# Kernel optimization log

Measured on AMD Instinct MI355X. Metric: run time of the kernel, lower is better.

Reference implementation:

```python
import jax, jax.numpy as jnp
import numpy as np

# Mamba2 dims (defaults: expand=2, d_state=128, d_conv=4, ngroups=1)
D_MODEL = 1024
HEADDIM = 64
D_STATE = 128
D_CONV = 4
D_INNER = 2 * D_MODEL            # 2048
NHEADS = D_INNER // HEADDIM      # 32
CONV_DIM = D_INNER + 2 * D_STATE # 2304
D_IN_PROJ = 2 * D_INNER + 2 * D_STATE + NHEADS  # 4384
EPS = 1e-5


def setup_inputs() -> dict:
    key = jax.random.key(0)
    ks = jax.random.split(key, 12)
    B, L = 4, 2048
    inp = {}
    inp['query'] = jax.random.normal(ks[0], (B, L, D_MODEL), jnp.float32)
    inp['key'] = jax.random.normal(ks[1], (B, L, D_MODEL), jnp.float32)
    inp['value'] = jax.random.normal(ks[2], (B, L, D_MODEL), jnp.float32)
    # parameters (Mamba2-style init)
    inp['in_proj_w'] = jax.random.normal(ks[3], (D_IN_PROJ, D_MODEL), jnp.float32) * (D_MODEL ** -0.5)
    inp['conv_w'] = jax.random.normal(ks[4], (CONV_DIM, D_CONV), jnp.float32) * (D_CONV ** -0.5)
    inp['conv_b'] = jnp.zeros((CONV_DIM,), jnp.float32)
    # dt init: softplus^{-1}(dt) with dt ~ U[1e-3, 1e-1]
    dt = jnp.exp(jax.random.uniform(ks[5], (NHEADS,)) * (np.log(0.1) - np.log(1e-3)) + np.log(1e-3))
    inp['dt_bias'] = dt + jnp.log(-jnp.expm1(-dt))
    # A ~ U[1, 16], A_log = log(A)
    inp['A_log'] = jnp.log(jax.random.uniform(ks[6], (NHEADS,), minval=1.0, maxval=16.0))
    inp['D'] = jnp.ones((NHEADS,), jnp.float32)
    inp['norm_w'] = jnp.ones((D_INNER,), jnp.float32)
    inp['out_proj_w'] = jax.random.normal(ks[7], (D_MODEL, D_INNER), jnp.float32) * (D_INNER ** -0.5)
    return inp


def _mamba2_forward(u, in_proj_w, conv_w, conv_b, dt_bias, A_log, D, norm_w, out_proj_w):
    b, l, _ = u.shape
    zxbcdt = jnp.einsum('bld,ed->ble', u, in_proj_w)  # (b,l,D_IN_PROJ)
    z = zxbcdt[..., :D_INNER]
    xBC = zxbcdt[..., D_INNER:D_INNER + CONV_DIM]
    dt = jax.nn.softplus(zxbcdt[..., -NHEADS:] + dt_bias)  # (b,l,h)
    # depthwise causal conv1d over time, kernel D_CONV, + silu
    xBC_pad = jnp.pad(xBC, ((0, 0), (D_CONV - 1, 0), (0, 0)))
    conv = conv_b
    for k in range(D_CONV):
        conv = conv + xBC_pad[:, k:k + l, :] * conv_w[:, k]
    xBC = jax.nn.silu(conv)
    x = xBC[..., :D_INNER].reshape(b, l, NHEADS, HEADDIM)   # (b,l,h,p)
    Bm = xBC[..., D_INNER:D_INNER + D_STATE]                # (b,l,n) ngroups=1
    Cm = xBC[..., D_INNER + D_STATE:]                       # (b,l,n)
    A = -jnp.exp(A_log)                                      # (h,)
    dA = jnp.exp(dt * A)                                     # (b,l,h)

    def step(h, inputs):
        dA_t, dt_t, x_t, B_t, C_t = inputs  # (b,h),(b,h),(b,h,p),(b,n),(b,n)
        h = h * dA_t[:, :, None, None] + (dt_t[:, :, None, None] * x_t[..., None]) * B_t[:, None, None, :]
        y = jnp.einsum('bhpn,bn->bhp', h, C_t)
        return h, y

    h0 = jnp.zeros((b, NHEADS, HEADDIM, D_STATE), u.dtype)
    xs = (dA.transpose(1, 0, 2), dt.transpose(1, 0, 2), x.transpose(1, 0, 2, 3),
          Bm.transpose(1, 0, 2), Cm.transpose(1, 0, 2))
    _, ys = jax.lax.scan(step, h0, xs)
    y = ys.transpose(1, 0, 2, 3) + x * D[None, None, :, None]  # (b,l,h,p)
    y = y.reshape(b, l, D_INNER)
    # RMSNormGated (norm_before_gate=False): norm(y * silu(z)) * w
    y = y * jax.nn.silu(z)
    y = y * jax.lax.rsqrt(jnp.mean(y * y, axis=-1, keepdims=True) + EPS) * norm_w
    return jnp.einsum('ble,de->bld', y, out_proj_w)


def reference(query, key, value, in_proj_w, conv_w, conv_b, dt_bias, A_log, D, norm_w, out_proj_w):
    # wrapper ignores key/value; returns mamba(query) (cache pass-through omitted)
    return _mamba2_forward(query, in_proj_w, conv_w, conv_b, dt_bias, A_log, D, norm_w, out_proj_w)
```

## Files before the change

### kernel.cpp

```cpp
#include <hip/hip_runtime.h>
#include <hip/hip_bf16.h>


typedef __attribute__((ext_vector_type(8))) short bf16x8;
typedef __attribute__((ext_vector_type(4))) float f32x4;

static constexpr int B_ = 4;
static constexpr int L_ = 2048;
static constexpr int NROWS = B_ * L_;
static constexpr int DMODEL = 1024;
static constexpr int DINNER = 2048;
static constexpr int NH = 32;
static constexpr int DSTATE = 128;
static constexpr int CONVDIM = DINNER + 2 * DSTATE;
static constexpr int DINPROJ = 2 * DINNER + 2 * DSTATE + NH;
static constexpr int Q_ = 64;
static constexpr int NCHUNK = L_ / Q_;

__device__ __forceinline__ unsigned pk_bf16(float a, float b) {
  unsigned ua = __builtin_bit_cast(unsigned, a);
  unsigned ub = __builtin_bit_cast(unsigned, b);
  ua = (ua + 0x7FFFu + ((ua >> 16) & 1u)) >> 16;
  ub = (ub + 0x7FFFu + ((ub >> 16) & 1u)) >> 16;
  return (ua & 0xFFFFu) | (ub << 16);
}
__device__ __forceinline__ unsigned short bf16_of(float a) {
  unsigned ua = __builtin_bit_cast(unsigned, a);
  return (unsigned short)((ua + 0x7FFFu + ((ua >> 16) & 1u)) >> 16);
}
__device__ __forceinline__ float f_of_bf16(unsigned short s) {
  return __builtin_bit_cast(float, (unsigned)s << 16);
}
__device__ __forceinline__ unsigned short* state_slot(unsigned short* lo,
                                                      unsigned short* hi,
                                                      int bh, int c) {
  int i = bh * NCHUNK + c;
  return (i < 2048) ? lo + (size_t)i * 8192 : hi + (size_t)(i - 2048) * 8192;
}

__global__ __launch_bounds__(256) void cast4_kernel(const float* __restrict__ in,
                                                    unsigned short* __restrict__ out) {
  int i = blockIdx.x * 256 + threadIdx.x;
  float4 v = ((const float4*)in)[i];
  ((uint2*)out)[i] = make_uint2(pk_bf16(v.x, v.y), pk_bf16(v.z, v.w));
}

#define WAITVM(N) asm volatile("s_waitcnt vmcnt(" #N ")" ::: "memory")

template <bool C_BF16>
__global__ __launch_bounds__(512, 2) void gemm256_kernel(
    const unsigned short* __restrict__ A, const unsigned short* __restrict__ Bw,
    void* __restrict__ Cp, int M, int N, int K, int lda, int ldb, int ldc) {
  (void)M;
  __shared__ unsigned short sA[4 * 256 * 32];
  __shared__ unsigned short sB[4 * 256 * 32];
  const int tid = threadIdx.x;
  const int w = tid >> 6;
  const int lane = tid & 63;
  const int quad = lane >> 4;
  const int r15 = lane & 15;

  const int NT = gridDim.x;
  const int nwg = NT * gridDim.y;
  const int orig = blockIdx.y * NT + blockIdx.x;
  const int qq = nwg >> 3, rm = nwg & 7;
  const int xcd = orig & 7, loc = orig >> 3;
  const int id = (xcd < rm ? xcd * (qq + 1) : rm * (qq + 1) + (xcd - rm) * qq) + loc;
  const int m0 = (id / NT) << 8;
  const int n0 = (id % NT) << 8;

  const int wm = w >> 2;
  const int wn = w & 3;

  const int srow = lane >> 2;
  const int sch = lane & 3;
  const int row0 = w * 32 + srow;
  const int row1 = row0 + 16;
  const int ca0 = (sch ^ ((row0 >> 1) & 3)) * 8;
  const int ca1 = (sch ^ ((row1 >> 1) & 3)) * 8;
  const int nslice = K >> 5;

  f32x4 acc[8][4];
#pragma unroll
  for (int i = 0; i < 8; ++i)
#pragma unroll
    for (int j = 0; j < 4; ++j) acc[i][j] = f32x4{0.f, 0.f, 0.f, 0.f};

  auto ldsA = (__attribute__((address_space(3))) unsigned short*)sA;
  auto ldsB = (__attribute__((address_space(3))) unsigned short*)sB;

  auto stage = [&](int ks) {
    const int so = (ks & 3) * 8192 + w * 1024;
    const unsigned short* ga = A + (size_t)(m0 + row0) * lda + ks * 32;
    const unsigned short* gb = Bw + (size_t)(n0 + row0) * ldb + ks * 32;
    __builtin_amdgcn_global_load_lds(
        (const __attribute__((address_space(1))) void*)(ga + ca0),
        (__attribute__((address_space(3))) void*)(ldsA + so), 16, 0, 0);
    __builtin_amdgcn_global_load_lds(
        (const __attribute__((address_space(1))) void*)(gb + ca0),
        (__attribute__((address_space(3))) void*)(ldsB + so), 16, 0, 0);
    __builtin_amdgcn_global_load_lds(
        (const __attribute__((address_space(1))) void*)(ga + (size_t)16 * lda + ca1),
        (__attribute__((address_space(3))) void*)(ldsA + so + 512), 16, 0, 0);
    __builtin_amdgcn_global_load_lds(
        (const __attribute__((address_space(1))) void*)(gb + (size_t)16 * ldb + ca1),
        (__attribute__((address_space(3))) void*)(ldsB + so + 512), 16, 0, 0);
  };

  stage(0);
  stage(1);
  stage(2);
  WAITVM(8);
  __builtin_amdgcn_s_barrier();

  const int kx = (quad ^ ((r15 >> 1) & 3)) * 8;
  int s = 0;

#define GPHASE(STAGE_STMT, WTN)                                                \
  {                                                                            \
    const unsigned short* pa = sA + (s & 3) * 8192;                            \
    const unsigned short* pb = sB + (s & 3) * 8192;                            \
    bf16x8 af[8], bfv[4];                                                      \
    _Pragma("unroll") for (int i = 0; i < 8; ++i)                              \
        af[i] = *(const bf16x8*)&pa[(wm * 128 + i * 16 + r15) * 32 + kx];      \
    _Pragma("unroll") for (int j = 0; j < 4; ++j)                              \
        bfv[j] = *(const bf16x8*)&pb[(wn * 64 + j * 16 + r15) * 32 + kx];      \
    STAGE_STMT;                                                                \
    WAITVM(WTN);                                                               \
    __builtin_amdgcn_s_barrier();                                              \
    __builtin_amdgcn_s_setprio(1);                                             \
    _Pragma("unroll") for (int i = 0; i < 8; ++i)                              \
        _Pragma("unroll") for (int j = 0; j < 4; ++j)                          \
            acc[i][j] = __builtin_amdgcn_mfma_f32_16x16x32_bf16(               \
                af[i], bfv[j], acc[i][j], 0, 0, 0);                            \
    __builtin_amdgcn_s_setprio(0);                                             \
    __builtin_amdgcn_s_barrier();                                              \
  }

  for (; s < nslice - 3; ++s) GPHASE(stage(s + 3), 8);
  GPHASE((void)0, 4);
  ++s;
  GPHASE((void)0, 0);
  ++s;
  GPHASE((void)0, 0);
#undef GPHASE

  const int rq = quad * 4;
#pragma unroll
  for (int i = 0; i < 8; ++i) {
#pragma unroll
    for (int j = 0; j < 4; ++j) {
      int gcol = n0 + wn * 64 + j * 16 + r15;
      if (gcol < N) {
#pragma unroll
        for (int r = 0; r < 4; ++r) {
          size_t grow = (size_t)(m0 + wm * 128 + i * 16 + rq + r);
          if constexpr (C_BF16)
            ((unsigned short*)Cp)[grow * (size_t)ldc + gcol] = bf16_of(acc[i][j][r]);
          else
            ((float*)Cp)[grow * (size_t)ldc + gcol] = acc[i][j][r];
        }
      }
    }
  }
}

__global__ __launch_bounds__(256) void conv_kernel(const unsigned short* __restrict__ zx,
                                                   const float* __restrict__ conv_w,
                                                   const float* __restrict__ conv_b,
                                                   unsigned short* __restrict__ xbc) {
  int c = blockIdx.x * 256 + threadIdx.x;
  int row = blockIdx.y;
  int l = row & (L_ - 1);
  float acc = conv_b[c];
#pragma unroll
  for (int k = 0; k < 4; ++k) {
    int ll = l + k - 3;
    if (ll >= 0)
      acc = fmaf(f_of_bf16(zx[(size_t)(row + k - 3) * DINPROJ + DINNER + c]),
                 conv_w[c * 4 + k], acc);
  }
  acc = acc / (1.f + __expf(-acc));
  xbc[(size_t)row * CONVDIM + c] = bf16_of(acc);
}

__global__ __launch_bounds__(256) void dt_kernel(const unsigned short* __restrict__ zx,
                                                 const float* __restrict__ dt_bias,
                                                 float* __restrict__ dtv) {
  int i = blockIdx.x * 256 + threadIdx.x;
  int hh = i & (NH - 1);
  int row = i >> 5;
  float x = f_of_bf16(zx[(size_t)row * DINPROJ + DINNER + CONVDIM + hh]) + dt_bias[hh];
  dtv[i] = (x > 20.f) ? x : log1pf(__expf(x));
}

__global__ __launch_bounds__(256) void ssd_passA(unsigned short* __restrict__ xbc,
                                                 const float* __restrict__ dtv,
                                                 const float* __restrict__ A_log,
                                                 const float* __restrict__ Dvec,
                                                 unsigned short* __restrict__ st_lo,
                                                 unsigned short* __restrict__ st_hi) {
  const int bid = blockIdx.x;
  const int h = bid & 31;
  const int c = (bid >> 5) & 31;
  const int b = bid >> 10;
  const int bh = b * 32 + h;
  const int tid = threadIdx.x;
  const int w = tid >> 6;
  const int lane = tid & 63;
  const int quad = lane >> 4;
  const int c15 = lane & 15;

  __shared__ unsigned short sXt[64 * 72];
  __shared__ unsigned short sBq[64 * 136];
  __shared__ unsigned short sCB[128 * 72];
  __shared__ float sdt[64], scs[64], sg[64];

  const float A = -__expf(A_log[h]);
  const float Dh = Dvec[h];
  const int r0 = b * L_ + c * Q_;

  if (w == 0) {
    float v = dtv[(size_t)(r0 + lane) * NH + h];
    sdt[lane] = v;
    float s = v;
#pragma unroll
    for (int off = 1; off < 64; off <<= 1) {
      float t = __shfl_up(s, off, 64);
      if (lane >= off) s += t;
    }
    scs[lane] = s;
    float T = __shfl(s, 63, 64);
    sg[lane] = __expf(A * (T - s)) * v;
  }
  for (int e = tid; e < 512; e += 256) {
    int t = e & 63, pb = e >> 6;
    uint4 v = *(const uint4*)&xbc[(size_t)(r0 + t) * CONVDIM + h * 64 + pb * 8];
    const unsigned short* sv = (const unsigned short*)&v;
#pragma unroll
    for (int j = 0; j < 8; ++j) sXt[(pb * 8 + j) * 72 + t] = sv[j];
  }
  for (int e = tid; e < 1024; e += 256) {
    int s = e >> 4, ch = e & 15;
    size_t roff = (size_t)(r0 + s) * CONVDIM + DINNER;
    *(uint4*)&sBq[s * 136 + ch * 8] = *(const uint4*)&xbc[roff + ch * 8];
    *(uint4*)&sCB[s * 136 + ch * 8] = *(const uint4*)&xbc[roff + DSTATE + ch * 8];
  }
  __syncthreads();

  const int wt = w >> 1, wx = w & 1;
  f32x4 sacc[2][2];
#pragma unroll
  for (int i = 0; i < 2; ++i)
#pragma unroll
    for (int j = 0; j < 2; ++j) sacc[i][j] = f32x4{0.f, 0.f, 0.f, 0.f};
#pragma unroll
  for (int kk = 0; kk < 4; ++kk) {
    int k8 = quad * 8 + kk * 32;
    bf16x8 a0 = *(const bf16x8*)&sCB[(wt * 32 + c15) * 136 + k8];
    bf16x8 a1 = *(const bf16x8*)&sCB[(wt * 32 + 16 + c15) * 136 + k8];
    bf16x8 b0 = *(const bf16x8*)&sBq[(wx * 32 + c15) * 136 + k8];
    bf16x8 b1 = *(const bf16x8*)&sBq[(wx * 32 + 16 + c15) * 136 + k8];
    sacc[0][0] = __builtin_amdgcn_mfma_f32_16x16x32_bf16(a0, b0, sacc[0][0], 0, 0, 0);
    sacc[0][1] = __builtin_amdgcn_mfma_f32_16x16x32_bf16(a0, b1, sacc[0][1], 0, 0, 0);
    sacc[1][0] = __builtin_amdgcn_mfma_f32_16x16x32_bf16(a1, b0, sacc[1][0], 0, 0, 0);
    sacc[1][1] = __builtin_amdgcn_mfma_f32_16x16x32_bf16(a1, b1, sacc[1][1], 0, 0, 0);
  }
  __syncthreads();

#pragma unroll
  for (int i = 0; i < 2; ++i)
#pragma unroll
    for (int j = 0; j < 2; ++j) {
      int scol = wx * 32 + j * 16 + c15;
      float css = scs[scol], dts = sdt[scol];
#pragma unroll
      for (int r = 0; r < 4; ++r) {
        int trow = wt * 32 + i * 16 + quad * 4 + r;
        float v = (scol <= trow) ? sacc[i][j][r] * __expf(A * (scs[trow] - css)) * dts : 0.f;
        sBq[trow * 72 + scol] = bf16_of(v);
      }
    }
  for (int e = tid; e < 1024; e += 256) {
    int s = e & 63, nb = e >> 6;
    uint4 v = *(const uint4*)&xbc[(size_t)(r0 + s) * CONVDIM + DINNER + nb * 8];
    float g = sg[s];
    const unsigned short* sv = (const unsigned short*)&v;
#pragma unroll
    for (int j = 0; j < 8; ++j)
      sCB[(nb * 8 + j) * 72 + s] = bf16_of(f_of_bf16(sv[j]) * g);
  }
  __syncthreads();

  f32x4 yacc[2][2];
#pragma unroll
  for (int i = 0; i < 2; ++i)
#pragma unroll
    for (int j = 0; j < 2; ++j) yacc[i][j] = f32x4{0.f, 0.f, 0.f, 0.f};
#pragma unroll
  for (int kk = 0; kk < 2; ++kk) {
    int k8 = quad * 8 + kk * 32;
    bf16x8 a0 = *(const bf16x8*)&sBq[(wt * 32 + c15) * 72 + k8];
    bf16x8 a1 = *(const bf16x8*)&sBq[(wt * 32 + 16 + c15) * 72 + k8];
    bf16x8 b0 = *(const bf16x8*)&sXt[(wx * 32 + c15) * 72 + k8];
    bf16x8 b1 = *(const bf16x8*)&sXt[(wx * 32 + 16 + c15) * 72 + k8];
    yacc[0][0] = __builtin_amdgcn_mfma_f32_16x16x32_bf16(a0, b0, yacc[0][0], 0, 0, 0);
    yacc[0][1] = __builtin_amdgcn_mfma_f32_16x16x32_bf16(a0, b1, yacc[0][1], 0, 0, 0);
    yacc[1][0] = __builtin_amdgcn_mfma_f32_16x16x32_bf16(a1, b0, yacc[1][0], 0, 0, 0);
    yacc[1][1] = __builtin_amdgcn_mfma_f32_16x16x32_bf16(a1, b1, yacc[1][1], 0, 0, 0);
  }
#pragma unroll
  for (int i = 0; i < 2; ++i)
#pragma unroll
    for (int j = 0; j < 2; ++j) {
      int p = wx * 32 + j * 16 + c15;
#pragma unroll
      for (int r = 0; r < 4; ++r) {
        int t = wt * 32 + i * 16 + quad * 4 + r;
        float xv = f_of_bf16(sXt[p * 72 + t]);
        xbc[(size_t)(r0 + t) * CONVDIM + h * 64 + p] = bf16_of(yacc[i][j][r] + Dh * xv);
      }
    }

  f32x4 hacc[2][4];
#pragma unroll
  for (int i = 0; i < 2; ++i)
#pragma unroll
    for (int j = 0; j < 4; ++j) hacc[i][j] = f32x4{0.f, 0.f, 0.f, 0.f};
  const int wp = w >> 1, wn = w & 1;
#pragma unroll
  for (int kk = 0; kk < 2; ++kk) {
    int k8 = quad * 8 + kk * 32;
    bf16x8 a0 = *(const bf16x8*)&sXt[(wp * 32 + c15) * 72 + k8];
    bf16x8 a1 = *(const bf16x8*)&sXt[(wp * 32 + 16 + c15) * 72 + k8];
    bf16x8 bfr[4];
#pragma unroll
    for (int j = 0; j < 4; ++j)
      bfr[j] = *(const bf16x8*)&sCB[(wn * 64 + j * 16 + c15) * 72 + k8];
#pragma unroll
    for (int j = 0; j < 4; ++j) {
      hacc[0][j] = __builtin_amdgcn_mfma_f32_16x16x32_bf16(a0, bfr[j], hacc[0][j], 0, 0, 0);
      hacc[1][j] = __builtin_amdgcn_mfma_f32_16x16x32_bf16(a1, bfr[j], hacc[1][j], 0, 0, 0);
    }
  }
  unsigned short* slot = state_slot(st_lo, st_hi, bh, c);
#pragma unroll
  for (int i = 0; i < 2; ++i)
#pragma unroll
    for (int j = 0; j < 4; ++j)
#pragma unroll
      for (int r = 0; r < 4; ++r) {
        int p = wp * 32 + i * 16 + quad * 4 + r;
        int n = wn * 64 + j * 16 + c15;
        slot[p * 128 + n] = bf16_of(hacc[i][j][r]);
      }
}

__global__ __launch_bounds__(256) void ssd_passB(const float* __restrict__ dtv,
                                                 const float* __restrict__ A_log,
                                                 unsigned short* __restrict__ st_lo,
                                                 unsigned short* __restrict__ st_hi) {
  const int bh = blockIdx.x >> 1;
  const int ph = blockIdx.x & 1;
  const int h = bh & 31;
  const int b = bh >> 5;
  const int tid = threadIdx.x;
  __shared__ float sd[NCHUNK];
  const float A = -__expf(A_log[h]);
  if (tid < NCHUNK) {
    float s = 0.f;
    const float* dp = dtv + (size_t)(b * L_ + tid * Q_) * NH + h;
    for (int i = 0; i < Q_; ++i) s += dp[(size_t)i * NH];
    sd[tid] = __expf(A * s);
  }
  __syncthreads();
  float hreg[16];
#pragma unroll
  for (int k = 0; k < 16; ++k) hreg[k] = 0.f;
  const size_t eoff = (size_t)ph * 4096 + (size_t)tid * 16;
  for (int c = 0; c < NCHUNK; ++c) {
    unsigned short* sp = state_slot(st_lo, st_hi, bh, c) + eoff;
    uint4 t0 = ((const uint4*)sp)[0];
    uint4 t1 = ((const uint4*)sp)[1];
    unsigned o[8];
#pragma unroll
    for (int k = 0; k < 8; ++k) o[k] = pk_bf16(hreg[2 * k], hreg[2 * k + 1]);
    ((uint4*)sp)[0] = make_uint4(o[0], o[1], o[2], o[3]);
    ((uint4*)sp)[1] = make_uint4(o[4], o[5], o[6], o[7]);
    float d = sd[c];
    const unsigned short* tv0 = (const unsigned short*)&t0;
    const unsigned short* tv1 = (const unsigned short*)&t1;
#pragma unroll
    for (int k = 0; k < 8; ++k) hreg[k] = d * hreg[k] + f_of_bf16(tv0[k]);
#pragma unroll
    for (int k = 0; k < 8; ++k) hreg[8 + k] = d * hreg[8 + k] + f_of_bf16(tv1[k]);
  }
}

__global__ __launch_bounds__(256) void ssd_passC(unsigned short* __restrict__ xbc,
                                                 const float* __restrict__ dtv,
                                                 const float* __restrict__ A_log,
                                                 const unsigned short* __restrict__ st_lo,
                                                 const unsigned short* __restrict__ st_hi) {
  const int bid = blockIdx.x;
  const int h = bid & 31;
  const int c = (bid >> 5) & 31;
  const int b = bid >> 10;
  const int bh = b * 32 + h;
  const int tid = threadIdx.x;
  const int w = tid >> 6;
  const int lane = tid & 63;
  const int quad = lane >> 4;
  const int c15 = lane & 15;

  __shared__ unsigned short sC[64 * 136];
  __shared__ unsigned short sH[64 * 136];
  __shared__ float srt[64];

  const float A = -__expf(A_log[h]);
  const int r0 = b * L_ + c * Q_;

  if (w == 0) {
    float v = dtv[(size_t)(r0 + lane) * NH + h];
    float s = v;
#pragma unroll
    for (int off = 1; off < 64; off <<= 1) {
      float t = __shfl_up(s, off, 64);
      if (lane >= off) s += t;
    }
    srt[lane] = __expf(A * s);
  }
  const unsigned short* slot =
      state_slot((unsigned short*)st_lo, (unsigned short*)st_hi, bh, c);
  for (int e = tid; e < 1024; e += 256) {
    int s = e >> 4, ch = e & 15;
    *(uint4*)&sC[s * 136 + ch * 8] =
        *(const uint4*)&xbc[(size_t)(r0 + s) * CONVDIM + DINNER + DSTATE + ch * 8];
    *(uint4*)&sH[s * 136 + ch * 8] = *(const uint4*)&slot[s * 128 + ch * 8];
  }
  __syncthreads();

  const int wt = w >> 1, wx = w & 1;
  f32x4 yacc[2][2];
#pragma unroll
  for (int i = 0; i < 2; ++i)
#pragma unroll
    for (int j = 0; j < 2; ++j) yacc[i][j] = f32x4{0.f, 0.f, 0.f, 0.f};
#pragma unroll
  for (int kk = 0; kk < 4; ++kk) {
    int k8 = quad * 8 + kk * 32;
    bf16x8 a0 = *(const bf16x8*)&sC[(wt * 32 + c15) * 136 + k8];
    bf16x8 a1 = *(const bf16x8*)&sC[(wt * 32 + 16 + c15) * 136 + k8];
    bf16x8 b0 = *(const bf16x8*)&sH[(wx * 32 + c15) * 136 + k8];
    bf16x8 b1 = *(const bf16x8*)&sH[(wx * 32 + 16 + c15) * 136 + k8];
    yacc[0][0] = __builtin_amdgcn_mfma_f32_16x16x32_bf16(a0, b0, yacc[0][0], 0, 0, 0);
    yacc[0][1] = __builtin_amdgcn_mfma_f32_16x16x32_bf16(a0, b1, yacc[0][1], 0, 0, 0);
    yacc[1][0] = __builtin_amdgcn_mfma_f32_16x16x32_bf16(a1, b0, yacc[1][0], 0, 0, 0);
    yacc[1][1] = __builtin_amdgcn_mfma_f32_16x16x32_bf16(a1, b1, yacc[1][1], 0, 0, 0);
  }
#pragma unroll
  for (int i = 0; i < 2; ++i)
#pragma unroll
    for (int j = 0; j < 2; ++j) {
      int p = wx * 32 + j * 16 + c15;
#pragma unroll
      for (int r = 0; r < 4; ++r) {
        int t = wt * 32 + i * 16 + quad * 4 + r;
        size_t ga = (size_t)(r0 + t) * CONVDIM + h * 64 + p;
        float v = yacc[i][j][r] * srt[t] + f_of_bf16(xbc[ga]);
        xbc[ga] = bf16_of(v);
      }
    }
}

__global__ __launch_bounds__(256) void norm_kernel(const unsigned short* __restrict__ y_in,
                                                   unsigned short* __restrict__ zxb,
                                                   const float* __restrict__ norm_w) {
  const int row = blockIdx.x;
  const int tid = threadIdx.x;
  float v[8];
  float ss = 0.f;
#pragma unroll
  for (int i = 0; i < 8; ++i) {
    int c = tid + i * 256;
    float yv = f_of_bf16(y_in[(size_t)row * CONVDIM + c]);
    float z = f_of_bf16(zxb[(size_t)row * DINPROJ + c]);
    yv *= z / (1.f + __expf(-z));
    v[i] = yv;
    ss = fmaf(yv, yv, ss);
  }
#pragma unroll
  for (int o = 32; o > 0; o >>= 1) ss += __shfl_down(ss, o, 64);
  __shared__ float sred[4];
  if ((tid & 63) == 0) sred[tid >> 6] = ss;
  __syncthreads();
  float tot = (sred[0] + sred[1]) + (sred[2] + sred[3]);
  float r = rsqrtf(tot * (1.f / (float)DINNER) + 1e-5f);
#pragma unroll
  for (int i = 0; i < 8; ++i) {
    int c = tid + i * 256;
    zxb[(size_t)row * DINPROJ + c] = bf16_of(v[i] * r * norm_w[c]);
  }
}

extern "C" void kernel_launch(void* const* d_in, const int* in_sizes, int n_in,
                              void* d_out, int out_size, void* d_ws, size_t ws_size,
                              hipStream_t stream) {
  (void)in_sizes; (void)n_in; (void)out_size;
  const float* u          = (const float*)d_in[0];
  const float* in_proj_w  = (const float*)d_in[3];
  const float* conv_w     = (const float*)d_in[4];
  const float* conv_b     = (const float*)d_in[5];
  const float* dt_bias    = (const float*)d_in[6];
  const float* A_log      = (const float*)d_in[7];
  const float* Dvec       = (const float*)d_in[8];
  const float* norm_w     = (const float*)d_in[9];
  const float* out_proj_w = (const float*)d_in[10];
  float* out = (float*)d_out;

  constexpr size_t SZ_ZX   = (size_t)NROWS * DINPROJ * 2;
  constexpr size_t SZ_XBC  = (size_t)NROWS * CONVDIM * 2;
  constexpr size_t SZ_DT   = (size_t)NROWS * NH * 4;
  constexpr size_t SZ_SHR  = 33554432;
  constexpr size_t SZ_WOUT = (size_t)DMODEL * DINNER * 2;
  constexpr size_t NEED = SZ_ZX + SZ_XBC + SZ_DT + SZ_SHR + SZ_WOUT;
  if (ws_size < NEED) return;

  char* p = (char*)d_ws;
  unsigned short* zxb  = (unsigned short*)p; p += SZ_ZX;
  unsigned short* xbc  = (unsigned short*)p; p += SZ_XBC;
  float* dtv           = (float*)p;          p += SZ_DT;
  char* shared_reg     = p;                  p += SZ_SHR;
  unsigned short* wout_bf = (unsigned short*)p;

  unsigned short* u_bf   = (unsigned short*)shared_reg;
  unsigned short* win_bf = (unsigned short*)(shared_reg + 16777216);
  unsigned short* st_lo  = (unsigned short*)d_out;
  unsigned short* st_hi  = (unsigned short*)shared_reg;

  cast4_kernel<<<(NROWS * DMODEL) / 1024, 256, 0, stream>>>(u, u_bf);
  cast4_kernel<<<(DINPROJ * DMODEL) / 1024, 256, 0, stream>>>(in_proj_w, win_bf);
  cast4_kernel<<<(DMODEL * DINNER) / 1024, 256, 0, stream>>>(out_proj_w, wout_bf);

  gemm256_kernel<true><<<dim3(18, 32), 512, 0, stream>>>(
      u_bf, win_bf, zxb, NROWS, DINPROJ, DMODEL, DMODEL, DMODEL, DINPROJ);
  conv_kernel<<<dim3(9, NROWS), 256, 0, stream>>>(zxb, conv_w, conv_b, xbc);
  dt_kernel<<<(NROWS * NH) / 256, 256, 0, stream>>>(zxb, dt_bias, dtv);

  ssd_passA<<<B_ * NCHUNK * NH, 256, 0, stream>>>(xbc, dtv, A_log, Dvec, st_lo, st_hi);
  ssd_passB<<<B_ * NH * 2, 256, 0, stream>>>(dtv, A_log, st_lo, st_hi);
  ssd_passC<<<B_ * NCHUNK * NH, 256, 0, stream>>>(xbc, dtv, A_log, st_lo, st_hi);

  norm_kernel<<<NROWS, 256, 0, stream>>>(xbc, zxb, norm_w);
  gemm256_kernel<false><<<dim3(4, 32), 512, 0, stream>>>(
      zxb, wout_bf, out, NROWS, DMODEL, DINNER, DINPROJ, DINNER, DMODEL);
}
```

Before: 510.3 us.

## Double-buffer LDS fragment reads in GEMM and use 128-row tiles for out_proj

Restructures the bf16 GEMM main loop so the LDS fragment reads for the next K slice are issued before the MFMAs of the current slice. Fragments ping-pong between two register sets, which removes one barrier per slice. A and B tiles now share one LDS buffer with a unified load loop. The tile height is templated, so the out_proj GEMM runs with BM=128 on twice as many workgroups for better occupancy. Launch bounds drop to one block per SIMD-pair hint, which raises register headroom but may reduce co-residency.

```diff
diff --git a/kernel.cpp b/kernel.cpp
--- a/kernel.cpp
+++ b/kernel.cpp
@@ -47,13 +47,16 @@
 
 #define WAITVM(N) asm volatile("s_waitcnt vmcnt(" #N ")" ::: "memory")
 
-template <bool C_BF16>
-__global__ __launch_bounds__(512, 2) void gemm256_kernel(
+template <int BM, bool C_BF16>
+__global__ __launch_bounds__(512, 1) void gemm256_kernel(
     const unsigned short* __restrict__ A, const unsigned short* __restrict__ Bw,
     void* __restrict__ Cp, int M, int N, int K, int lda, int ldb, int ldc) {
   (void)M;
-  __shared__ unsigned short sA[4 * 256 * 32];
-  __shared__ unsigned short sB[4 * 256 * 32];
+  constexpr int MI = BM / 32;
+  constexpr int TOTROWS = BM + 256;
+  constexpr int RPW = TOTROWS / 8;
+  constexpr int NLD = RPW / 16;
+  __shared__ unsigned short sAB[4 * TOTROWS * 32];
   const int tid = threadIdx.x;
   const int w = tid >> 6;
   const int lane = tid & 63;
@@ -66,95 +69,103 @@
   const int qq = nwg >> 3, rm = nwg & 7;
   const int xcd = orig & 7, loc = orig >> 3;
   const int id = (xcd < rm ? xcd * (qq + 1) : rm * (qq + 1) + (xcd - rm) * qq) + loc;
-  const int m0 = (id / NT) << 8;
-  const int n0 = (id % NT) << 8;
+  const int m0 = (id / NT) * BM;
+  const int n0 = (id % NT) * 256;
 
   const int wm = w >> 2;
   const int wn = w & 3;
 
-  const int srow = lane >> 2;
-  const int sch = lane & 3;
-  const int row0 = w * 32 + srow;
-  const int row1 = row0 + 16;
-  const int ca0 = (sch ^ ((row0 >> 1) & 3)) * 8;
-  const int ca1 = (sch ^ ((row1 >> 1) & 3)) * 8;
+  const unsigned short* gsrc[NLD];
+  int lofs[NLD];
+#pragma unroll
+  for (int ld = 0; ld < NLD; ++ld) {
+    int r16 = w * RPW + ld * 16;
+    int row = r16 + (lane >> 2);
+    int ca = ((lane & 3) ^ ((row >> 1) & 3)) * 8;
+    gsrc[ld] = (r16 < BM) ? A + (size_t)(m0 + row) * lda + ca
+                          : Bw + (size_t)(n0 + row - BM) * ldb + ca;
+    lofs[ld] = r16 * 32;
+  }
   const int nslice = K >> 5;
 
-  f32x4 acc[8][4];
-#pragma unroll
-  for (int i = 0; i < 8; ++i)
+  f32x4 acc[MI][4];
+#pragma unroll
+  for (int i = 0; i < MI; ++i)
 #pragma unroll
     for (int j = 0; j < 4; ++j) acc[i][j] = f32x4{0.f, 0.f, 0.f, 0.f};
 
-  auto ldsA = (__attribute__((address_space(3))) unsigned short*)sA;
-  auto ldsB = (__attribute__((address_space(3))) unsigned short*)sB;
+  auto ldsAB = (__attribute__((address_space(3))) unsigned short*)sAB;
 
   auto stage = [&](int ks) {
-    const int so = (ks & 3) * 8192 + w * 1024;
-    const unsigned short* ga = A + (size_t)(m0 + row0) * lda + ks * 32;
-    const unsigned short* gb = Bw + (size_t)(n0 + row0) * ldb + ks * 32;
-    __builtin_amdgcn_global_load_lds(
-        (const __attribute__((address_space(1))) void*)(ga + ca0),
-        (__attribute__((address_space(3))) void*)(ldsA + so), 16, 0, 0);
-    __builtin_amdgcn_global_load_lds(
-        (const __attribute__((address_space(1))) void*)(gb + ca0),
-        (__attribute__((address_space(3))) void*)(ldsB + so), 16, 0, 0);
-    __builtin_amdgcn_global_load_lds(
-        (const __attribute__((address_space(1))) void*)(ga + (size_t)16 * lda + ca1),
-        (__attribute__((address_space(3))) void*)(ldsA + so + 512), 16, 0, 0);
-    __builtin_amdgcn_global_load_lds(
-        (const __attribute__((address_space(1))) void*)(gb + (size_t)16 * ldb + ca1),
-        (__attribute__((address_space(3))) void*)(ldsB + so + 512), 16, 0, 0);
+    const int so = (ks & 3) * (TOTROWS * 32);
+#pragma unroll
+    for (int ld = 0; ld < NLD; ++ld)
+      __builtin_amdgcn_global_load_lds(
+          (const __attribute__((address_space(1))) void*)(gsrc[ld] + (size_t)ks * 32),
+          (__attribute__((address_space(3))) void*)(ldsAB + so + lofs[ld]), 16, 0, 0);
   };
+
+  const int kx = (quad ^ ((r15 >> 1) & 3)) * 8;
+
+  bf16x8 a0[MI], b0[4], a1[MI], b1[4];
+
+#define READF(S, AV, BV)                                                        \
+  {                                                                             \
+    const int so_ = ((S) & 3) * (TOTROWS * 32);                                 \
+    _Pragma("unroll") for (int i = 0; i < MI; ++i)                              \
+        AV[i] = *(const bf16x8*)&sAB[so_ + (wm * (BM / 2) + i * 16 + r15) * 32 + kx]; \
+    _Pragma("unroll") for (int j = 0; j < 4; ++j)                               \
+        BV[j] = *(const bf16x8*)&sAB[so_ + (BM + wn * 64 + j * 16 + r15) * 32 + kx];  \
+  }
+#define MFMAC(AV, BV)                                                           \
+  _Pragma("unroll") for (int i = 0; i < MI; ++i)                                \
+      _Pragma("unroll") for (int j = 0; j < 4; ++j)                             \
+          acc[i][j] = __builtin_amdgcn_mfma_f32_16x16x32_bf16(AV[i], BV[j],     \
+                                                              acc[i][j], 0, 0, 0);
 
   stage(0);
   stage(1);
   stage(2);
-  WAITVM(8);
+  if constexpr (NLD == 4) WAITVM(4); else WAITVM(3);
   __builtin_amdgcn_s_barrier();
-
-  const int kx = (quad ^ ((r15 >> 1) & 3)) * 8;
-  int s = 0;
-
-#define GPHASE(STAGE_STMT, WTN)                                                \
-  {                                                                            \
-    const unsigned short* pa = sA + (s & 3) * 8192;                            \
-    const unsigned short* pb = sB + (s & 3) * 8192;                            \
-    bf16x8 af[8], bfv[4];                                                      \
-    _Pragma("unroll") for (int i = 0; i < 8; ++i)                              \
-        af[i] = *(const bf16x8*)&pa[(wm * 128 + i * 16 + r15) * 32 + kx];      \
-    _Pragma("unroll") for (int j = 0; j < 4; ++j)                              \
-        bfv[j] = *(const bf16x8*)&pb[(wn * 64 + j * 16 + r15) * 32 + kx];      \
-    STAGE_STMT;                                                                \
-    WAITVM(WTN);                                                               \
-    __builtin_amdgcn_s_barrier();                                              \
-    __builtin_amdgcn_s_setprio(1);                                             \
-    _Pragma("unroll") for (int i = 0; i < 8; ++i)                              \
-        _Pragma("unroll") for (int j = 0; j < 4; ++j)                          \
-            acc[i][j] = __builtin_amdgcn_mfma_f32_16x16x32_bf16(               \
-                af[i], bfv[j], acc[i][j], 0, 0, 0);                            \
-    __builtin_amdgcn_s_setprio(0);                                             \
-    __builtin_amdgcn_s_barrier();                                              \
-  }
-
-  for (; s < nslice - 3; ++s) GPHASE(stage(s + 3), 8);
-  GPHASE((void)0, 4);
-  ++s;
-  GPHASE((void)0, 0);
-  ++s;
-  GPHASE((void)0, 0);
-#undef GPHASE
+  __builtin_amdgcn_sched_barrier(0);
+  READF(0, a0, b0);
+
+#define HALF(SS, CA, CB, NA, NB)                                                \
+  {                                                                             \
+    if ((SS) + 3 < nslice) stage((SS) + 3);                                     \
+    if ((SS) + 1 < nslice) READF((SS) + 1, NA, NB);                             \
+    __builtin_amdgcn_sched_barrier(0);                                          \
+    __builtin_amdgcn_s_setprio(1);                                              \
+    MFMAC(CA, CB);                                                              \
+    __builtin_amdgcn_s_setprio(0);                                              \
+    if ((SS) + 3 < nslice) {                                                    \
+      if constexpr (NLD == 4) WAITVM(4); else WAITVM(3);                        \
+    } else {                                                                    \
+      WAITVM(0);                                                                \
+    }                                                                           \
+    __builtin_amdgcn_s_barrier();                                               \
+    __builtin_amdgcn_sched_barrier(0);                                          \
+  }
+
+  for (int s = 0; s < nslice; s += 2) {
+    HALF(s, a0, b0, a1, b1);
+    HALF(s + 1, a1, b1, a0, b0);
+  }
+#undef HALF
+#undef MFMAC
+#undef READF
 
   const int rq = quad * 4;
 #pragma unroll
-  for (int i = 0; i < 8; ++i) {
+  for (int i = 0; i < MI; ++i) {
 #pragma unroll
     for (int j = 0; j < 4; ++j) {
       int gcol = n0 + wn * 64 + j * 16 + r15;
       if (gcol < N) {
 #pragma unroll
         for (int r = 0; r < 4; ++r) {
-          size_t grow = (size_t)(m0 + wm * 128 + i * 16 + rq + r);
+          size_t grow = (size_t)(m0 + wm * (BM / 2) + i * 16 + rq + r);
           if constexpr (C_BF16)
             ((unsigned short*)Cp)[grow * (size_t)ldc + gcol] = bf16_of(acc[i][j][r]);
           else
@@ -542,7 +553,7 @@
   cast4_kernel<<<(DINPROJ * DMODEL) / 1024, 256, 0, stream>>>(in_proj_w, win_bf);
   cast4_kernel<<<(DMODEL * DINNER) / 1024, 256, 0, stream>>>(out_proj_w, wout_bf);
 
-  gemm256_kernel<true><<<dim3(18, 32), 512, 0, stream>>>(
+  gemm256_kernel<256, true><<<dim3(18, 32), 512, 0, stream>>>(
       u_bf, win_bf, zxb, NROWS, DINPROJ, DMODEL, DMODEL, DMODEL, DINPROJ);
   conv_kernel<<<dim3(9, NROWS), 256, 0, stream>>>(zxb, conv_w, conv_b, xbc);
   dt_kernel<<<(NROWS * NH) / 256, 256, 0, stream>>>(zxb, dt_bias, dtv);
@@ -552,6 +563,6 @@
   ssd_passC<<<B_ * NCHUNK * NH, 256, 0, stream>>>(xbc, dtv, A_log, st_lo, st_hi);
 
   norm_kernel<<<NROWS, 256, 0, stream>>>(xbc, zxb, norm_w);
-  gemm256_kernel<false><<<dim3(4, 32), 512, 0, stream>>>(
+  gemm256_kernel<128, false><<<dim3(4, 64), 512, 0, stream>>>(
       zxb, wout_bf, out, NROWS, DMODEL, DINNER, DINPROJ, DINNER, DMODEL);
 }
```

Result: faster. 485.3 us (-4.9%).
